# Optimization experiments

Measured on AMD Instinct MI355X. Metric: run time of the kernel, lower is better.

The kernel has to match this reference:

```python
import jax, jax.numpy as jnp
import numpy as np

B, CDD, HIS, S, L, F, K = 32, 5, 100, 20, 3, 150, 18
NNEWS, RDIM = 10000, 256


def _maxpool3(x):
    # kernel [3,3,3], stride [3,3,3], no padding (torch MaxPool3d default)
    return jax.lax.reduce_window(x, -jnp.inf, jax.lax.max,
                                 (1, 1, 3, 3, 3), (1, 1, 3, 3, 3), 'VALID')


def setup_inputs() -> dict:
    key = jax.random.key(0)
    ks = jax.random.split(key, 10)
    return {
        'cdd_id': jax.random.randint(ks[0], (B, CDD), 0, NNEWS),
        'his_id': jax.random.randint(ks[1], (B, HIS), 0, NNEWS),
        'news_repr_table': jax.random.normal(ks[2], (NNEWS, RDIM), jnp.float32),
        'news_embedding_table': jax.random.normal(ks[3], (NNEWS, S * L * F), jnp.float32),
        'conv1_w': jax.random.normal(ks[4], (32, 3, 3, 3, 3), jnp.float32) * 0.1,
        'conv1_b': jax.random.normal(ks[5], (32,), jnp.float32) * 0.1,
        'conv2_w': jax.random.normal(ks[6], (16, 32, 3, 3, 3), jnp.float32) * 0.1,
        'conv2_b': jax.random.normal(ks[7], (16,), jnp.float32) * 0.1,
        'ltr_w': jax.random.normal(ks[8], (1, 128), jnp.float32) * 0.1,
        'ltr_b': jax.random.normal(ks[9], (1,), jnp.float32) * 0.1,
    }


def reference(cdd_id, his_id, news_repr_table, news_embedding_table,
              conv1_w, conv1_b, conv2_w, conv2_b, ltr_w, ltr_b):
    cdd_repr = news_repr_table[cdd_id]                    # [B,CDD,R]
    his_repr = news_repr_table[his_id]                    # [B,HIS,R]
    cdd_emb = news_embedding_table[cdd_id].reshape(B, CDD, S, L, F)
    his_emb = news_embedding_table[his_id]                # [B,HIS,S*L*F]

    # attention scores; original applies softmax then sorts the (detached)
    # weights -- softmax is monotone per row so argsort on logits is identical
    attn = jnp.einsum('bcr,bhr->bch', cdd_repr, his_repr)  # [B,CDD,HIS]
    topk_idx = jnp.argsort(-attn, axis=-1)[..., :K]        # [B,CDD,K]

    # direct gather (replaces the one_hot @ embedding matmul, same math)
    his_act = his_emb[jnp.arange(B)[:, None, None], topk_idx]  # [B,CDD,K,S*L*F]
    his_act = his_act.reshape(B, CDD, K, S, L, F)

    # fusion tensor at each dilation level
    cdd_t = cdd_emb.transpose(0, 1, 3, 2, 4)       # [B,CDD,L,S,F]
    his_t = his_act.transpose(0, 1, 2, 4, 3, 5)    # [B,CDD,K,L,S,F]
    fusion = jnp.einsum('bclsf,bckltf->bcklst', cdd_t, his_t) / np.sqrt(F).astype(np.float32)
    x = fusion.reshape(B * CDD, K, L, S, S).transpose(0, 2, 1, 3, 4)  # [B*CDD,L,K,S,S]

    dn = ('NCDHW', 'OIDHW', 'NCDHW')
    pad1 = [(1, 1)] * 3
    x = jax.lax.conv_general_dilated(x, conv1_w, (1, 1, 1), pad1, dimension_numbers=dn)
    x = jax.nn.relu(x + conv1_b[None, :, None, None, None])
    x = _maxpool3(x)                                # [B*CDD,32,6,6,6]
    x = jax.lax.conv_general_dilated(x, conv2_w, (1, 1, 1), pad1, dimension_numbers=dn)
    x = jax.nn.relu(x + conv2_b[None, :, None, None, None])
    x = _maxpool3(x)                                # [B*CDD,16,2,2,2]

    feat = x.reshape(B, CDD, -1)                    # [B,CDD,128]
    score = jnp.einsum('bcd,od->bco', feat, ltr_w)[..., 0] + ltr_b[0]  # [B,CDD]
    return jax.nn.log_softmax(score, axis=1)
```

## Files before the change

### kernel.cpp

```cpp
#include <hip/hip_runtime.h>
#include <hip/hip_bf16.h>
#include <math.h>

#define B_    32
#define CDD_  5
#define HIS_  100
#define S_    20
#define L_    3
#define F_    150
#define K_    18
#define RDIM_ 256
#define ROWE_ 9000
#define NBC_  160

__global__ __launch_bounds__(256) void prep_kernel(
    const float* __restrict__ w1, const float* __restrict__ w2,
    float* __restrict__ w1t, float* __restrict__ w2t) {
  int tid = blockIdx.x * 256 + threadIdx.x;
  if (tid < 32 * 81) {
    int oc = tid / 81, j = tid % 81;
    w1t[j * 32 + oc] = w1[tid];
  }
  if (tid < 16 * 864) {
    int oc = tid / 864, r = tid % 864;
    w2t[r * 16 + oc] = w2[tid];
  }
}

__global__ __launch_bounds__(256) void attn_topk_kernel(
    const int* __restrict__ cdd_id, const int* __restrict__ his_id,
    const float* __restrict__ repr, int* __restrict__ gid,
    float* __restrict__ score) {
  int bc = blockIdx.x;
  int b  = bc / CDD_;
  int tid = threadIdx.x, lane = tid & 63, wave = tid >> 6;
  __shared__ float cddv[RDIM_];
  __shared__ float sattn[128];
  int cid = cdd_id[bc];
  cddv[tid] = repr[(size_t)cid * RDIM_ + tid];
  if (tid < 28) sattn[100 + tid] = -INFINITY;
  __syncthreads();

  float4 cv = *(const float4*)(cddv + lane * 4);
  for (int h = wave; h < HIS_; h += 4) {
    const float4* row = (const float4*)(repr + (size_t)his_id[b * HIS_ + h] * RDIM_);
    float4 rv = row[lane];
    float p = cv.x * rv.x;
    p = fmaf(cv.y, rv.y, p);
    p = fmaf(cv.z, rv.z, p);
    p = fmaf(cv.w, rv.w, p);
    #pragma unroll
    for (int off = 32; off >= 1; off >>= 1) p += __shfl_xor(p, off);
    if (lane == 0) sattn[h] = p;
  }
  __syncthreads();

  if (wave == 0) {
    float v0 = sattn[lane], v1 = sattn[lane + 64];
    for (int k = 0; k < K_; k++) {
      float bv; int bi;
      if (v1 > v0) { bv = v1; bi = lane + 64; } else { bv = v0; bi = lane; }
      #pragma unroll
      for (int off = 32; off >= 1; off >>= 1) {
        float ov = __shfl_xor(bv, off);
        int   oi = __shfl_xor(bi, off);
        if (ov > bv || (ov == bv && oi < bi)) { bv = ov; bi = oi; }
      }
      if (lane == 0) gid[bc * K_ + k] = his_id[b * HIS_ + bi];
      if (bi == lane)      v0 = -INFINITY;
      if (bi == lane + 64) v1 = -INFINITY;
    }
  }
  if (tid == 0) score[bc] = 0.f;
}

__global__ __launch_bounds__(256) void fusion_kernel(
    const int* __restrict__ cdd_id, const int* __restrict__ gid,
    const float* __restrict__ emb, float* __restrict__ x1) {
  int bck = blockIdx.x;
  int bc = bck / K_, k = bck % K_;
  __shared__ float hs[ROWE_];
  const float* crow = emb + (size_t)cdd_id[bc] * ROWE_;
  const float4* h4 = (const float4*)(emb + (size_t)gid[bck] * ROWE_);
  float4* hs4 = (float4*)hs;
  for (int i = threadIdx.x; i < ROWE_ / 4; i += 256) hs4[i] = h4[i];
  __syncthreads();

  const float scale = 0.0816496580927726f;
  for (int tile = threadIdx.x; tile < 300; tile += 256) {
    int l = tile / 100; int rem = tile % 100;
    int s0 = (rem / 10) * 2, t0 = (rem % 10) * 2;
    const float* c0 = crow + s0 * 450 + l * 150;
    const float* c1 = c0 + 450;
    const float* h0 = hs + t0 * 450 + l * 150;
    const float* h1 = h0 + 450;
    float a00 = 0, a01 = 0, a10 = 0, a11 = 0;
    for (int f = 0; f < F_; f += 2) {
      float2 ca = *(const float2*)(c0 + f);
      float2 cb = *(const float2*)(c1 + f);
      float2 ha = *(const float2*)(h0 + f);
      float2 hb = *(const float2*)(h1 + f);
      a00 = fmaf(ca.x, ha.x, a00); a00 = fmaf(ca.y, ha.y, a00);
      a01 = fmaf(ca.x, hb.x, a01); a01 = fmaf(ca.y, hb.y, a01);
      a10 = fmaf(cb.x, ha.x, a10); a10 = fmaf(cb.y, ha.y, a10);
      a11 = fmaf(cb.x, hb.x, a11); a11 = fmaf(cb.y, hb.y, a11);
    }
    size_t base = ((size_t)(bc * 3 + l) * K_ + k) * 400 + s0 * 20 + t0;
    x1[base]      = a00 * scale;
    x1[base + 1]  = a01 * scale;
    x1[base + 20] = a10 * scale;
    x1[base + 21] = a11 * scale;
  }
}

__global__ __launch_bounds__(256) void conv1_kernel(
    const float* __restrict__ x1, const float* __restrict__ w1t,
    const float* __restrict__ b1, float* __restrict__ p1) {
  int bid = blockIdx.x;
  int n = bid / 6, dp = bid % 6;
  __shared__ float tile[3 * 5 * 22 * 22];
  __shared__ unsigned pooled[32 * 36];
  int tid = threadIdx.x;

  for (int i = tid; i < 7260; i += 256) {
    int c = i / 2420; int r = i % 2420;
    int dd = r / 484; r %= 484;
    int hh = r / 22, ww = r % 22;
    int d = dp * 3 + dd - 1, h = hh - 1, w = ww - 1;
    float v = 0.f;
    if (d >= 0 && d < 18 && h >= 0 && h < 20 && w >= 0 && w < 20)
      v = x1[((size_t)(n * 3 + c) * K_ + d) * 400 + h * 20 + w];
    tile[i] = v;
  }
  for (int i = tid; i < 1152; i += 256) pooled[i] = 0u;
  __syncthreads();

  for (int pos = tid; pos < 972; pos += 256) {
    int dl = pos / 324; int r = pos % 324;
    int h = r / 18, w = r % 18;
    float acc[32];
    #pragma unroll
    for (int oc = 0; oc < 32; oc++) acc[oc] = b1[oc];

    for (int c = 0; c < 3; c++) {
      const float* tc = tile + (c * 5 + dl) * 484 + h * 22 + w;
      const float* wc = w1t + c * 27 * 32;
      #pragma unroll
      for (int kd = 0; kd < 3; kd++)
        #pragma unroll
        for (int kh = 0; kh < 3; kh++)
          #pragma unroll
          for (int kw = 0; kw < 3; kw++) {
            float iv = tc[kd * 484 + kh * 22 + kw];
            const float* wp = wc + (kd * 9 + kh * 3 + kw) * 32;
            #pragma unroll
            for (int oc = 0; oc < 32; oc++) acc[oc] = fmaf(iv, wp[oc], acc[oc]);
          }
    }
    int pbase = (h / 3) * 6 + (w / 3);
    #pragma unroll
    for (int oc = 0; oc < 32; oc++)
      atomicMax(&pooled[oc * 36 + pbase], __float_as_uint(fmaxf(acc[oc], 0.f)));
  }
  __syncthreads();
  for (int i = tid; i < 1152; i += 256) {
    int oc = i / 36; int r = i % 36;
    p1[(size_t)(n * 32 + oc) * 216 + dp * 36 + r] = __uint_as_float(pooled[i]);
  }
}

__global__ __launch_bounds__(256) void conv2_kernel(
    const float* __restrict__ p1, const float* __restrict__ w2t,
    const float* __restrict__ b2, const float* __restrict__ lw,
    float* __restrict__ score) {
  int bid = blockIdx.x;
  int n = bid / 2, og = bid % 2;
  __shared__ float tile[32 * 8 * 8 * 8];
  __shared__ unsigned pooled[64];
  int tid = threadIdx.x;

  for (int i = tid; i < 32 * 512; i += 256) tile[i] = 0.f;
  if (tid < 64) pooled[tid] = 0u;
  __syncthreads();
  for (int i = tid; i < 32 * 216; i += 256) {
    int c = i / 216; int r = i % 216;
    int d = r / 36; r %= 36;
    int h = r / 6, w = r % 6;
    tile[c * 512 + (d + 1) * 64 + (h + 1) * 8 + (w + 1)] =
        p1[(size_t)n * 32 * 216 + i];
  }
  __syncthreads();

  if (tid < 216) {
    int d = tid / 36; int r = tid % 36;
    int h = r / 6, w = r % 6;
    float acc[8];
    #pragma unroll
    for (int oc = 0; oc < 8; oc++) acc[oc] = b2[og * 8 + oc];
    for (int c = 0; c < 32; c++) {
      const float* tc = tile + c * 512 + d * 64 + h * 8 + w;
      const float* wc = w2t + c * 27 * 16 + og * 8;
      #pragma unroll
      for (int kd = 0; kd < 3; kd++)
        #pragma unroll
        for (int kh = 0; kh < 3; kh++)
          #pragma unroll
          for (int kw = 0; kw < 3; kw++) {
            float iv = tc[kd * 64 + kh * 8 + kw];
            const float* wp = wc + (kd * 9 + kh * 3 + kw) * 16;
            #pragma unroll
            for (int oc = 0; oc < 8; oc++) acc[oc] = fmaf(iv, wp[oc], acc[oc]);
          }
    }
    int pb = (d / 3) * 4 + (h / 3) * 2 + (w / 3);
    #pragma unroll
    for (int oc = 0; oc < 8; oc++)
      atomicMax(&pooled[oc * 8 + pb], __float_as_uint(fmaxf(acc[oc], 0.f)));
  }
  __syncthreads();

  if (tid < 64) {
    int oc = tid / 8, pb = tid % 8;
    float contrib = __uint_as_float(pooled[tid]) * lw[(og * 8 + oc) * 8 + pb];
    #pragma unroll
    for (int off = 32; off >= 1; off >>= 1) contrib += __shfl_xor(contrib, off);
    if (tid == 0) atomicAdd(&score[n], contrib);
  }
}

__global__ __launch_bounds__(64) void softmax_kernel(
    const float* __restrict__ score, const float* __restrict__ lb,
    float* __restrict__ out) {
  int b = threadIdx.x;
  if (b < B_) {
    float s[CDD_];
    float mx = -INFINITY;
    #pragma unroll
    for (int c = 0; c < CDD_; c++) {
      s[c] = score[b * CDD_ + c] + lb[0];
      mx = fmaxf(mx, s[c]);
    }
    float sum = 0.f;
    #pragma unroll
    for (int c = 0; c < CDD_; c++) sum += expf(s[c] - mx);
    float lse = mx + logf(sum);
    #pragma unroll
    for (int c = 0; c < CDD_; c++) out[b * CDD_ + c] = s[c] - lse;
  }
}

extern "C" void kernel_launch(void* const* d_in, const int* in_sizes, int n_in,
                              void* d_out, int out_size, void* d_ws, size_t ws_size,
                              hipStream_t stream) {
  const int*   cdd_id = (const int*)d_in[0];
  const int*   his_id = (const int*)d_in[1];
  const float* repr   = (const float*)d_in[2];
  const float* emb    = (const float*)d_in[3];
  const float* w1     = (const float*)d_in[4];
  const float* b1     = (const float*)d_in[5];
  const float* w2     = (const float*)d_in[6];
  const float* b2     = (const float*)d_in[7];
  const float* lw     = (const float*)d_in[8];
  const float* lb     = (const float*)d_in[9];
  float* out = (float*)d_out;

  char* ws = (char*)d_ws;
  int*   gid   = (int*)ws;
  float* score = (float*)(ws + 11520);
  float* x1    = (float*)(ws + 12160);
  float* p1    = (float*)(ws + 12160 + 13824000);
  float* w1t   = (float*)(ws + 12160 + 13824000 + 4423680);
  float* w2t   = (float*)(ws + 12160 + 13824000 + 4423680 + 10368);

  prep_kernel<<<54, 256, 0, stream>>>(w1, w2, w1t, w2t);
  attn_topk_kernel<<<NBC_, 256, 0, stream>>>(cdd_id, his_id, repr, gid, score);
  fusion_kernel<<<NBC_ * K_, 256, 0, stream>>>(cdd_id, gid, emb, x1);
  conv1_kernel<<<NBC_ * 6, 256, 0, stream>>>(x1, w1t, b1, p1);
  conv2_kernel<<<NBC_ * 2, 256, 0, stream>>>(p1, w2t, b2, lw, score);
  softmax_kernel<<<1, 64, 0, stream>>>(score, lb, out);
}
```

Measured before the change: 623.5 us.

## Compute fusion tensor with bf16 MFMA and fold weight prep into attention kernel

Rewrites the fusion kernel so that both the candidate and the history embedding rows are converted to bf16 into zero-padded shared-memory tiles (32x160 per dilation level). The S x S products are then computed with 16x16x32 bf16 MFMA instructions instead of scalar FP32 FMAs. Separately, the weight-transpose prep kernel is merged into the attention/top-k kernel to remove one launch. This trades FP32 accuracy for bf16 inputs, which risks tolerance failures downstream, and adds the shared-memory zeroing and conversion work.

After: 613.0 us. No clear change (-1.7%).

```diff
diff --git a/kernel.cpp b/kernel.cpp
--- a/kernel.cpp
+++ b/kernel.cpp
@@ -13,27 +13,35 @@
 #define ROWE_ 9000
 #define NBC_  160
 
-__global__ __launch_bounds__(256) void prep_kernel(
-    const float* __restrict__ w1, const float* __restrict__ w2,
-    float* __restrict__ w1t, float* __restrict__ w2t) {
-  int tid = blockIdx.x * 256 + threadIdx.x;
-  if (tid < 32 * 81) {
-    int oc = tid / 81, j = tid % 81;
-    w1t[j * 32 + oc] = w1[tid];
-  }
-  if (tid < 16 * 864) {
-    int oc = tid / 864, r = tid % 864;
-    w2t[r * 16 + oc] = w2[tid];
-  }
+typedef __attribute__((ext_vector_type(8))) short short8;
+typedef __attribute__((ext_vector_type(4))) float f32x4;
+
+static __device__ __forceinline__ unsigned short f2bf(float x) {
+  union { float f; unsigned u; } v; v.f = x;
+  unsigned r = v.u + 0x7fffu + ((v.u >> 16) & 1u);
+  return (unsigned short)(r >> 16);
 }
 
 __global__ __launch_bounds__(256) void attn_topk_kernel(
     const int* __restrict__ cdd_id, const int* __restrict__ his_id,
     const float* __restrict__ repr, int* __restrict__ gid,
-    float* __restrict__ score) {
+    float* __restrict__ score,
+    const float* __restrict__ w1, const float* __restrict__ w2,
+    float* __restrict__ w1t, float* __restrict__ w2t) {
   int bc = blockIdx.x;
   int b  = bc / CDD_;
   int tid = threadIdx.x, lane = tid & 63, wave = tid >> 6;
+
+  int gidx = bc * 256 + tid;
+  if (gidx < 2592) {
+    int oc = gidx / 81, j = gidx % 81;
+    w1t[j * 32 + oc] = w1[gidx];
+  } else if (gidx < 2592 + 13824) {
+    int i2 = gidx - 2592;
+    int oc = i2 / 864, r = i2 % 864;
+    w2t[r * 16 + oc] = w2[i2];
+  }
+
   __shared__ float cddv[RDIM_];
   __shared__ float sattn[128];
   int cid = cdd_id[bc];
@@ -79,37 +87,52 @@
     const float* __restrict__ emb, float* __restrict__ x1) {
   int bck = blockIdx.x;
   int bc = bck / K_, k = bck % K_;
-  __shared__ float hs[ROWE_];
+  __shared__ unsigned short a_sh[3 * 32 * 160];
+  __shared__ unsigned short b_sh[3 * 32 * 160];
+  int tid = threadIdx.x;
+
+  unsigned* az = (unsigned*)a_sh;
+  unsigned* bz = (unsigned*)b_sh;
+  for (int i = tid; i < 3 * 32 * 80; i += 256) { az[i] = 0u; bz[i] = 0u; }
+  __syncthreads();
+
   const float* crow = emb + (size_t)cdd_id[bc] * ROWE_;
-  const float4* h4 = (const float4*)(emb + (size_t)gid[bck] * ROWE_);
-  float4* hs4 = (float4*)hs;
-  for (int i = threadIdx.x; i < ROWE_ / 4; i += 256) hs4[i] = h4[i];
-  __syncthreads();
-
+  const float* hrow = emb + (size_t)gid[bck] * ROWE_;
+  for (int p = tid; p < 4500; p += 256) {
+    int s = p / 225, r = p % 225;
+    int l = r / 75, f2 = r % 75;
+    int src = s * 450 + l * 150 + 2 * f2;
+    float2 cv = *(const float2*)(crow + src);
+    float2 hv = *(const float2*)(hrow + src);
+    int dst = (l * 32 + s) * 80 + f2;
+    az[dst] = (unsigned)f2bf(cv.x) | ((unsigned)f2bf(cv.y) << 16);
+    bz[dst] = (unsigned)f2bf(hv.x) | ((unsigned)f2bf(hv.y) << 16);
+  }
+  __syncthreads();
+
+  int wave = tid >> 6, lane = tid & 63;
+  int m15 = lane & 15, quad = lane >> 4;
   const float scale = 0.0816496580927726f;
-  for (int tile = threadIdx.x; tile < 300; tile += 256) {
-    int l = tile / 100; int rem = tile % 100;
-    int s0 = (rem / 10) * 2, t0 = (rem % 10) * 2;
-    const float* c0 = crow + s0 * 450 + l * 150;
-    const float* c1 = c0 + 450;
-    const float* h0 = hs + t0 * 450 + l * 150;
-    const float* h1 = h0 + 450;
-    float a00 = 0, a01 = 0, a10 = 0, a11 = 0;
-    for (int f = 0; f < F_; f += 2) {
-      float2 ca = *(const float2*)(c0 + f);
-      float2 cb = *(const float2*)(c1 + f);
-      float2 ha = *(const float2*)(h0 + f);
-      float2 hb = *(const float2*)(h1 + f);
-      a00 = fmaf(ca.x, ha.x, a00); a00 = fmaf(ca.y, ha.y, a00);
-      a01 = fmaf(ca.x, hb.x, a01); a01 = fmaf(ca.y, hb.y, a01);
-      a10 = fmaf(cb.x, ha.x, a10); a10 = fmaf(cb.y, ha.y, a10);
-      a11 = fmaf(cb.x, hb.x, a11); a11 = fmaf(cb.y, hb.y, a11);
-    }
-    size_t base = ((size_t)(bc * 3 + l) * K_ + k) * 400 + s0 * 20 + t0;
-    x1[base]      = a00 * scale;
-    x1[base + 1]  = a01 * scale;
-    x1[base + 20] = a10 * scale;
-    x1[base + 21] = a11 * scale;
+  for (int j = wave; j < 12; j += 4) {
+    int l = j >> 2, mt = (j >> 1) & 1, nt = j & 1;
+    f32x4 acc = {0.f, 0.f, 0.f, 0.f};
+    int abase = (l * 32 + mt * 16 + m15) * 160 + quad * 8;
+    int bbase = (l * 32 + nt * 16 + m15) * 160 + quad * 8;
+    #pragma unroll
+    for (int kb = 0; kb < 5; kb++) {
+      short8 af = *(const short8*)(a_sh + abase + kb * 32);
+      short8 bf = *(const short8*)(b_sh + bbase + kb * 32);
+      acc = __builtin_amdgcn_mfma_f32_16x16x32_bf16(af, bf, acc, 0, 0, 0);
+    }
+    int t = nt * 16 + m15;
+    if (t < 20) {
+      size_t base = ((size_t)(bc * 3 + l) * K_ + k) * 400;
+      #pragma unroll
+      for (int reg = 0; reg < 4; reg++) {
+        int s = mt * 16 + quad * 4 + reg;
+        if (s < 20) x1[base + s * 20 + t] = acc[reg] * scale;
+      }
+    }
   }
 }
 
@@ -272,8 +295,8 @@
   float* w1t   = (float*)(ws + 12160 + 13824000 + 4423680);
   float* w2t   = (float*)(ws + 12160 + 13824000 + 4423680 + 10368);
 
-  prep_kernel<<<54, 256, 0, stream>>>(w1, w2, w1t, w2t);
-  attn_topk_kernel<<<NBC_, 256, 0, stream>>>(cdd_id, his_id, repr, gid, score);
+  attn_topk_kernel<<<NBC_, 256, 0, stream>>>(cdd_id, his_id, repr, gid, score,
+                                             w1, w2, w1t, w2t);
   fusion_kernel<<<NBC_ * K_, 256, 0, stream>>>(cdd_id, gid, emb, x1);
   conv1_kernel<<<NBC_ * 6, 256, 0, stream>>>(x1, w1t, b1, p1);
   conv2_kernel<<<NBC_ * 2, 256, 0, stream>>>(p1, w2t, b2, lw, score);
```
